# Kernel tuning notes

Hardware: AMD Instinct MI355X
Metric: run time of the kernel (lower is better)

## Reference

```python
import jax, jax.numpy as jnp
import numpy as np

N_NODES = 50000
BN_EPS = 1e-5


def gcn_conv(x, W, b, src, dst):
    # PyG GCNConv: linear, add self-loops, symmetric degree normalization, scatter-add, bias.
    h = x @ W                                        # [N, D]
    n = x.shape[0]
    deg = jax.ops.segment_sum(jnp.ones(src.shape[0], x.dtype), dst,
                              num_segments=n) + 1.0  # +1 for self-loop
    dinv = jnp.where(deg > 0, jax.lax.rsqrt(deg), 0.0)
    norm = dinv[src] * dinv[dst]                     # [E]
    agg = jax.ops.segment_sum(h[src] * norm[:, None], dst, num_segments=n)
    agg = agg + h * (dinv * dinv)[:, None]           # self-loop contribution
    return agg + b


def batch_norm(x, gamma, beta):
    # training-mode BN over the node axis (biased variance, as torch)
    mu = jnp.mean(x, axis=0)
    var = jnp.mean((x - mu) ** 2, axis=0)
    return (x - mu) * jax.lax.rsqrt(var + BN_EPS) * gamma + beta


def setup_inputs() -> dict:
    key = jax.random.key(0)
    ks = jax.random.split(key, 8)
    D, C = 128, 10
    x = jax.random.normal(ks[0], (N_NODES, D), dtype=jnp.float32)
    edge_index = jax.random.randint(ks[1], (2, 640000), 0, N_NODES, dtype=jnp.int32)
    s = 1.0 / np.sqrt(D)
    return {
        "x": x,
        "edge_index": edge_index,
        "W1": jax.random.normal(ks[2], (D, D), dtype=jnp.float32) * s,
        "b1": jnp.zeros((D,), jnp.float32),
        "gamma1": jnp.ones((D,), jnp.float32),
        "beta1": jnp.zeros((D,), jnp.float32),
        "W2": jax.random.normal(ks[3], (D, D), dtype=jnp.float32) * s,
        "b2": jnp.zeros((D,), jnp.float32),
        "gamma2": jnp.ones((D,), jnp.float32),
        "beta2": jnp.zeros((D,), jnp.float32),
        "lin1_w": jax.random.normal(ks[4], (D, D), dtype=jnp.float32) * s,
        "lin1_b": jnp.zeros((D,), jnp.float32),
        "lin2_w": jax.random.normal(ks[5], (D, C), dtype=jnp.float32) * s,
        "lin2_b": jnp.zeros((C,), jnp.float32),
    }


def reference(x, edge_index, W1, b1, gamma1, beta1, W2, b2, gamma2, beta2,
              lin1_w, lin1_b, lin2_w, lin2_b):
    src, dst = edge_index[0], edge_index[1]
    # layer 1: GCNConv -> ReLU -> BN (dropout = identity at eval)
    h = jax.nn.relu(gcn_conv(x, W1, b1, src, dst))
    h = batch_norm(h, gamma1, beta1)
    # layer 2
    h = jax.nn.relu(gcn_conv(h, W2, b2, src, dst))
    h = batch_norm(h, gamma2, beta2)
    # MLP head
    h = jax.nn.relu(h @ lin1_w + lin1_b)
    logits = h @ lin2_w + lin2_b
    return jax.nn.log_softmax(logits, axis=-1)
```

## Files before the change

kernel.cpp:

```cpp
#include <hip/hip_runtime.h>
#include <hip/hip_bf16.h>
#include <math.h>

typedef unsigned int uint;
typedef unsigned short ushort;
using f32x4 = __attribute__((ext_vector_type(4))) float;
using s16x8 = __attribute__((ext_vector_type(8))) short;

#define NSLOT 64

__device__ __forceinline__ float bflo(uint u) { return __uint_as_float(u << 16); }
__device__ __forceinline__ float bfhi(uint u) { return __uint_as_float(u & 0xffff0000u); }
__device__ __forceinline__ ushort f2bf(float f) {
    uint u = __float_as_uint(f);
    return (ushort)((u + 0x7fffu + ((u >> 16) & 1u)) >> 16);
}
__device__ __forceinline__ float sel4f(float a, float b, float c, float d, int i) {
    float r = a; r = (i == 1) ? b : r; r = (i == 2) ? c : r; r = (i == 3) ? d : r; return r;
}
__device__ __forceinline__ int sel4i(int a, int b, int c, int d, int i) {
    int r = a; r = (i == 1) ? b : r; r = (i == 2) ? c : r; r = (i == 3) ? d : r; return r;
}


__global__ __launch_bounds__(256) void init_prep(uint4* __restrict__ zbase, int nz, int ZB,
                                                 const float* __restrict__ W1,
                                                 const float* __restrict__ W2,
                                                 const float* __restrict__ W3,
                                                 const float* __restrict__ l2w,
                                                 const float* __restrict__ l2b,
                                                 ushort* __restrict__ wt1,
                                                 ushort* __restrict__ wt2,
                                                 ushort* __restrict__ wt3,
                                                 ushort* __restrict__ w2bf,
                                                 float* __restrict__ b2pad) {
    int bid = blockIdx.x;
    if (bid < ZB) {
        int i = bid * 256 + threadIdx.x;
        if (i < nz) zbase[i] = (uint4){0u, 0u, 0u, 0u};
        return;
    }
    int i = (bid - ZB) * 256 + threadIdx.x;
    int li = i & 16383;
    int k = li >> 7, n = li & 127;
    const float* Ws = (i < 16384) ? W1 : (i < 32768) ? W2 : W3;
    ushort* Wd = (i < 16384) ? wt1 : (i < 32768) ? wt2 : wt3;
    Wd[n * 128 + k] = f2bf(Ws[li]);
    if (i < 2048) {
        int c = i >> 7, kk = i & 127;
        float v = (c < 10) ? l2w[kk * 10 + c] : 0.f;
        w2bf[c * 128 + kk] = f2bf(v);
    }
    if (i < 16) b2pad[i] = (i < 10) ? l2b[i] : -1e30f;
}


__global__ __launch_bounds__(256) void deg_count(const int* __restrict__ dst,
                                                 int* __restrict__ deg, int E) {
    int base = blockIdx.x * 1024 + threadIdx.x;
    int d[4]; bool ok[4];
    #pragma unroll
    for (int k = 0; k < 4; ++k) {
        int e = base + k * 256;
        ok[k] = e < E;
        d[k] = ok[k] ? dst[e] : 0;
    }
    #pragma unroll
    for (int k = 0; k < 4; ++k)
        if (ok[k]) atomicAdd(&deg[d[k]], 1);
}


__global__ __launch_bounds__(256) void scan_fill(const int* __restrict__ deg,
                                                 int* __restrict__ bsum,
                                                 int* __restrict__ sync_ctr,
                                                 int* __restrict__ row_start,
                                                 int* __restrict__ cursor,
                                                 float* __restrict__ dinv,
                                                 int N, int E, int nblk) {
    __shared__ int s[256];
    __shared__ int sb[256];
    int t = threadIdx.x;
    int bid = blockIdx.x;
    int i = bid * 256 + t;
    int dg = (i < N) ? deg[i] : 0;
    s[t] = dg;
    __syncthreads();
    for (int off = 1; off < 256; off <<= 1) {
        int v = (t >= off) ? s[t - off] : 0;
        __syncthreads();
        s[t] += v;
        __syncthreads();
    }
    if (t == 0) {
        bsum[bid] = s[255];
        __threadfence();
        atomicAdd(sync_ctr, 1);
        while (atomicAdd(sync_ctr, 0) < nblk) __builtin_amdgcn_s_sleep(8);
    }
    __syncthreads();
    sb[t] = (t < nblk) ? atomicAdd(&bsum[t], 0) : 0;
    __syncthreads();
    for (int off = 1; off < 256; off <<= 1) {
        int v = (t >= off) ? sb[t - off] : 0;
        __syncthreads();
        sb[t] += v;
        __syncthreads();
    }
    if (i < N) {
        int boff = (bid == 0) ? 0 : sb[bid - 1];
        int excl = boff + s[t] - dg;
        row_start[i] = excl;
        cursor[i] = excl;
        dinv[i] = rsqrtf((float)dg + 1.0f);
    }
    if (i == 0) row_start[N] = E;
}


__global__ __launch_bounds__(256) void csr_fill(const int* __restrict__ src,
                                                const int* __restrict__ dst,
                                                int* __restrict__ cursor,
                                                int* __restrict__ csr_src, int E) {
    int base = blockIdx.x * 1024 + threadIdx.x;
    int s[4], d[4]; bool ok[4];
    #pragma unroll
    for (int k = 0; k < 4; ++k) {
        int e = base + k * 256;
        ok[k] = e < E;
        s[k] = ok[k] ? src[e] : 0;
        d[k] = ok[k] ? dst[e] : 0;
    }
    #pragma unroll
    for (int k = 0; k < 4; ++k) {
        if (ok[k]) {
            int p = atomicAdd(&cursor[d[k]], 1);
            csr_src[p] = s[k];
        }
    }
}


template<bool XF32, bool AFF, bool PRESCALE, bool HEAD>
__global__ __launch_bounds__(256) void gemm_mfma(const void* __restrict__ Xv,
                                                 const float* __restrict__ scale,
                                                 const float* __restrict__ shift,
                                                 const ushort* __restrict__ Bt,
                                                 const float* __restrict__ bias,
                                                 const float* __restrict__ dinv,
                                                 ushort* __restrict__ Y,
                                                 const ushort* __restrict__ W2bf,
                                                 const float* __restrict__ b2pad,
                                                 float* __restrict__ OUT, int N) {
    __shared__ char smem[2 * 16384 + 32768];
    char* Bl = smem + 32768;

    int tid = threadIdx.x;
    int brow = blockIdx.x * 128;

    {
        int n = tid >> 1, h = tid & 1;
        const uint4* srcp = (const uint4*)(Bt + n * 128 + h * 64);
        #pragma unroll
        for (int i = 0; i < 8; ++i) {
            uint4 v = srcp[i];
            int u = (h * 8 + i) ^ (n & 7);
            *(uint4*)(Bl + n * 256 + u * 16) = v;
        }
    }

    int lane = tid & 63, w = tid >> 6;
    int m = lane & 15, g = lane >> 4;
    int wr = w * 16;

    #pragma unroll
    for (int t = 0; t < 2; ++t) {
        char* Al = smem + t * 16384;
        int rbase = brow + t * 64;

        {
            int r = tid >> 2, c0 = (tid & 3) * 32;
            int row = rbase + r;
            bool ok = row < N;
            uint pk[16];
            if (XF32) {
                const float* Xr = (const float*)Xv + (size_t)row * 128 + c0;
                #pragma unroll
                for (int i = 0; i < 16; ++i) {
                    float f0 = ok ? Xr[i * 2] : 0.f;
                    float f1 = ok ? Xr[i * 2 + 1] : 0.f;
                    pk[i] = (uint)f2bf(f0) | ((uint)f2bf(f1) << 16);
                }
            } else {
                const uint* Xr = (const uint*)((const ushort*)Xv + (size_t)row * 128 + c0);
                #pragma unroll
                for (int i = 0; i < 16; ++i) {
                    uint u = ok ? Xr[i] : 0u;
                    float f0 = bflo(u), f1 = bfhi(u);
                    if (AFF) {
                        int c = c0 + i * 2;
                        f0 = f0 * scale[c] + shift[c];
                        f1 = f1 * scale[c + 1] + shift[c + 1];
                    }
                    pk[i] = (uint)f2bf(f0) | ((uint)f2bf(f1) << 16);
                }
            }
            #pragma unroll
            for (int i = 0; i < 4; ++i) {
                int u = ((tid & 3) * 4 + i) ^ (r & 7);
                *(uint4*)(Al + r * 256 + u * 16) = *(uint4*)&pk[i * 4];
            }
        }
        __syncthreads();

        f32x4 acc[8];
        #pragma unroll
        for (int nt = 0; nt < 8; ++nt) acc[nt] = (f32x4){0.f, 0.f, 0.f, 0.f};

        #pragma unroll
        for (int kk = 0; kk < 4; ++kk) {
            int u = (kk * 4 + g) ^ (m & 7);
            s16x8 a = *(const s16x8*)(Al + (wr + m) * 256 + u * 16);
            #pragma unroll
            for (int nt = 0; nt < 8; ++nt) {
                s16x8 b = *(const s16x8*)(Bl + (nt * 16 + m) * 256 + u * 16);
                acc[nt] = __builtin_amdgcn_mfma_f32_16x16x32_bf16(a, b, acc[nt], 0, 0, 0);
            }
        }

        if (!HEAD) {
            #pragma unroll
            for (int i = 0; i < 4; ++i) {
                int row = rbase + wr + g * 4 + i;
                if (row < N) {
                    float dv = PRESCALE ? dinv[row] : 1.f;
                    #pragma unroll
                    for (int nt = 0; nt < 8; ++nt) {
                        float v = acc[nt][i];
                        if (PRESCALE) v *= dv;
                        Y[(size_t)row * 128 + nt * 16 + m] = f2bf(v);
                    }
                }
            }
        } else {
            float bv[8];
            #pragma unroll
            for (int nt = 0; nt < 8; ++nt) bv[nt] = bias[nt * 16 + m];
            #pragma unroll
            for (int i = 0; i < 4; ++i) {
                int r = wr + g * 4 + i;
                #pragma unroll
                for (int nt = 0; nt < 8; ++nt) {
                    float v = fmaxf(acc[nt][i] + bv[nt], 0.f);
                    int col = nt * 16 + m;
                    int u = (col >> 3) ^ (r & 7);
                    *(ushort*)(Al + r * 256 + u * 16 + (col & 7) * 2) = f2bf(v);
                }
            }
            __syncthreads();
            float b2v = b2pad[m];
            f32x4 lg = (f32x4){b2v, b2v, b2v, b2v};
            #pragma unroll
            for (int kk = 0; kk < 4; ++kk) {
                int u = (kk * 4 + g) ^ (m & 7);
                s16x8 a = *(const s16x8*)(Al + (wr + m) * 256 + u * 16);
                s16x8 b = *(const s16x8*)(&W2bf[m * 128 + (kk * 4 + g) * 8]);
                lg = __builtin_amdgcn_mfma_f32_16x16x32_bf16(a, b, lg, 0, 0, 0);
            }
            #pragma unroll
            for (int i = 0; i < 4; ++i) {
                float v = lg[i];
                float mx = v;
                #pragma unroll
                for (int off = 8; off > 0; off >>= 1) mx = fmaxf(mx, __shfl_xor(mx, off, 64));
                float ex = expf(v - mx);
                float sm = ex;
                #pragma unroll
                for (int off = 8; off > 0; off >>= 1) sm += __shfl_xor(sm, off, 64);
                float res = v - (mx + logf(sm));
                int grow = rbase + wr + g * 4 + i;
                if (m < 10 && grow < N) OUT[(size_t)grow * 10 + m] = res;
            }
        }
    }
}


__global__ __launch_bounds__(256) void gather_fused(const ushort* __restrict__ H,
                                                    const int* __restrict__ row_start,
                                                    const int* __restrict__ csr_src,
                                                    const float* __restrict__ dinv,
                                                    const float* __restrict__ bias,
                                                    ushort* __restrict__ Y,
                                                    float* __restrict__ bnpart, int N) {
    int g = threadIdx.x >> 6, lane = threadIdx.x & 63;
    int d = lane * 2;
    float b0 = bias[d], b1 = bias[d + 1];
    float s0 = 0.f, s1 = 0.f, ss0 = 0.f, ss1 = 0.f;

    int nchunks = (N + 3) / 4;
    int chunk = blockIdx.x * 4 + g;

    if (chunk < nchunks) {
        int c = chunk * 4;
        int nn = min(4, N - c);

        int rsv = row_start[c + min(lane, nn)];
        int rs0 = __shfl(rsv, 0);
        int rs1 = __shfl(rsv, min(1, nn));
        int rs2 = __shfl(rsv, min(2, nn));
        int rs3 = __shfl(rsv, min(3, nn));
        int rs4 = __shfl(rsv, nn);

        float dvv = dinv[c + min(lane, nn - 1)];
        float dv0 = __shfl(dvv, 0);
        float dv1 = __shfl(dvv, min(1, nn - 1));
        float dv2 = __shfl(dvv, min(2, nn - 1));
        float dv3 = __shfl(dvv, min(3, nn - 1));

        uint h0 = *(const uint*)&H[(size_t)c * 128 + d];
        uint h1 = (nn > 1) ? *(const uint*)&H[(size_t)(c + 1) * 128 + d] : 0u;
        uint h2 = (nn > 2) ? *(const uint*)&H[(size_t)(c + 2) * 128 + d] : 0u;
        uint h3 = (nn > 3) ? *(const uint*)&H[(size_t)(c + 3) * 128 + d] : 0u;

        float i0_0 = bflo(h0) * dv0 + b0, i1_0 = bfhi(h0) * dv0 + b1;
        float i0_1 = bflo(h1) * dv1 + b0, i1_1 = bfhi(h1) * dv1 + b1;
        float i0_2 = bflo(h2) * dv2 + b0, i1_2 = bfhi(h2) * dv2 + b1;
        float i0_3 = bflo(h3) * dv3 + b0, i1_3 = bfhi(h3) * dv3 + b1;

        int e0 = rs0, eend = rs4;
        int seg = 0;
        int nextb = rs1;
        float i0s = i0_0, i1s = i1_0, dvs = dv0;
        float es0 = 0.f, es1 = 0.f;

        for (int base = e0; base < eend; base += 64) {
            int cnt = min(64, eend - base);
            int sl = (lane < cnt) ? csr_src[base + lane] : 0;

            for (int j = 0; j < cnt; j += 16) {
                int mm = min(16, cnt - j);
                uint v[16];
                #pragma unroll
                for (int k = 0; k < 16; ++k) {
                    int idx = min(j + k, cnt - 1);
                    int sk = __shfl(sl, idx);
                    v[k] = *(const uint*)&H[(size_t)sk * 128 + d];
                }
                #pragma unroll
                for (int k = 0; k < 16; ++k) {
                    if (k < mm) {
                        int e = base + j + k;
                        while (e >= nextb) {
                            float r0 = fmaxf(es0 * dvs + i0s, 0.f);
                            float r1 = fmaxf(es1 * dvs + i1s, 0.f);
                            *(uint*)&Y[(size_t)(c + seg) * 128 + d] =
                                (uint)f2bf(r0) | ((uint)f2bf(r1) << 16);
                            s0 += r0; ss0 += r0 * r0; s1 += r1; ss1 += r1 * r1;
                            seg++;
                            i0s = sel4f(i0_0, i0_1, i0_2, i0_3, seg);
                            i1s = sel4f(i1_0, i1_1, i1_2, i1_3, seg);
                            dvs = sel4f(dv0, dv1, dv2, dv3, seg);
                            nextb = sel4i(rs1, rs2, rs3, rs4, seg);
                            es0 = 0.f; es1 = 0.f;
                        }
                        es0 += bflo(v[k]);
                        es1 += bfhi(v[k]);
                    }
                }
            }
        }
        for (;;) {
            float r0 = fmaxf(es0 * dvs + i0s, 0.f);
            float r1 = fmaxf(es1 * dvs + i1s, 0.f);
            *(uint*)&Y[(size_t)(c + seg) * 128 + d] = (uint)f2bf(r0) | ((uint)f2bf(r1) << 16);
            s0 += r0; ss0 += r0 * r0; s1 += r1; ss1 += r1 * r1;
            seg++;
            if (seg >= nn) break;
            i0s = sel4f(i0_0, i0_1, i0_2, i0_3, seg);
            i1s = sel4f(i1_0, i1_1, i1_2, i1_3, seg);
            dvs = sel4f(dv0, dv1, dv2, dv3, seg);
            nextb = sel4i(rs1, rs2, rs3, rs4, seg);
            es0 = 0.f; es1 = 0.f;
        }
    }

    float* bp = bnpart + (size_t)(blockIdx.x & (NSLOT - 1)) * 256;
    __shared__ float red[4][128];
    red[g][d] = s0; red[g][d + 1] = s1;
    __syncthreads();
    if (g == 0) {
        atomicAdd(&bp[d],     red[0][d] + red[1][d] + red[2][d] + red[3][d]);
        atomicAdd(&bp[d + 1], red[0][d + 1] + red[1][d + 1] + red[2][d + 1] + red[3][d + 1]);
    }
    __syncthreads();
    red[g][d] = ss0; red[g][d + 1] = ss1;
    __syncthreads();
    if (g == 0) {
        atomicAdd(&bp[128 + d],     red[0][d] + red[1][d] + red[2][d] + red[3][d]);
        atomicAdd(&bp[128 + d + 1], red[0][d + 1] + red[1][d + 1] + red[2][d + 1] + red[3][d + 1]);
    }
}

__global__ void bnfinalize(float* __restrict__ bnpart,
                           const float* __restrict__ gamma, const float* __restrict__ beta,
                           float* __restrict__ scale, float* __restrict__ shift, float invN) {
    int d = threadIdx.x;
    float sum = 0.f, ss = 0.f;
    #pragma unroll 8
    for (int s = 0; s < NSLOT; ++s) {
        sum += bnpart[s * 256 + d];
        ss  += bnpart[s * 256 + 128 + d];
        bnpart[s * 256 + d] = 0.f;
        bnpart[s * 256 + 128 + d] = 0.f;
    }
    float mu  = sum * invN;
    float var = ss * invN - mu * mu;
    float sc  = gamma[d] * rsqrtf(var + 1e-5f);
    scale[d] = sc;
    shift[d] = beta[d] - mu * sc;
}


static inline char* align16(char* p) { return (char*)(((uintptr_t)p + 15) & ~(uintptr_t)15); }

extern "C" void kernel_launch(void* const* d_in, const int* in_sizes, int n_in,
                              void* d_out, int out_size, void* d_ws, size_t ws_size,
                              hipStream_t stream) {
    const float* x    = (const float*)d_in[0];
    const int*   ei   = (const int*)d_in[1];
    const float* W1   = (const float*)d_in[2];
    const float* b1   = (const float*)d_in[3];
    const float* g1   = (const float*)d_in[4];
    const float* be1  = (const float*)d_in[5];
    const float* W2   = (const float*)d_in[6];
    const float* b2   = (const float*)d_in[7];
    const float* g2   = (const float*)d_in[8];
    const float* be2  = (const float*)d_in[9];
    const float* l1w  = (const float*)d_in[10];
    const float* l1b  = (const float*)d_in[11];
    const float* l2w  = (const float*)d_in[12];
    const float* l2b  = (const float*)d_in[13];
    float* out = (float*)d_out;

    int N = in_sizes[0] / 128;
    int E = in_sizes[1] / 2;
    const int* srcp = ei;
    const int* dstp = ei + E;

    char* w = (char*)d_ws;
    ushort* bufA   = (ushort*)w;  w = align16(w + (size_t)N * 128 * 2);
    ushort* bufB   = (ushort*)w;  w = align16(w + (size_t)N * 128 * 2);
    char* zstart   = w;
    int*   degc    = (int*)w;     w += (size_t)N * 4;
    float* bnpart  = (float*)w;   w += (size_t)NSLOT * 256 * 4;
    int*   ctrs    = (int*)w;     w += 16;
    size_t zbytes  = (size_t)(w - zstart);
    w = align16(w);
    float* dinv    = (float*)w;   w = align16(w + (size_t)N * 4);
    int*   row_st  = (int*)w;     w = align16(w + (size_t)(N + 1) * 4);
    int*   cursor  = (int*)w;     w = align16(w + (size_t)N * 4);
    int*   bsum    = (int*)w;     w = align16(w + 256 * 4);
    int*   csr_src = (int*)w;     w = align16(w + (size_t)E * 4);
    float* scale   = (float*)w;   w = align16(w + 128 * 4);
    float* shift   = (float*)w;   w = align16(w + 128 * 4);
    ushort* wt1    = (ushort*)w;  w = align16(w + 16384 * 2);
    ushort* wt2    = (ushort*)w;  w = align16(w + 16384 * 2);
    ushort* wt3    = (ushort*)w;  w = align16(w + 16384 * 2);
    ushort* w2bf   = (ushort*)w;  w = align16(w + 2048 * 2);
    float* b2pad   = (float*)w;   w = align16(w + 16 * 4);

    int nz = (int)(zbytes / 16);
    int ZB = (nz + 255) / 256;
    int eg4 = (E + 1023) / 1024;
    int ng = (N + 255) / 256;
    int gemm_grid = (N + 127) / 128;
    int nchunks = (N + 3) / 4;
    int gather_grid = (nchunks + 3) / 4;
    float invN = 1.0f / (float)N;

    init_prep<<<ZB + 192, 256, 0, stream>>>((uint4*)zstart, nz, ZB,
                                            W1, W2, l1w, l2w, l2b, wt1, wt2, wt3, w2bf, b2pad);
    deg_count<<<eg4, 256, 0, stream>>>(dstp, degc, E);
    scan_fill<<<ng, 256, 0, stream>>>(degc, bsum, &ctrs[0], row_st, cursor, dinv, N, E, ng);
    csr_fill<<<eg4, 256, 0, stream>>>(srcp, dstp, cursor, csr_src, E);

    gemm_mfma<true, false, true, false><<<gemm_grid, 256, 0, stream>>>(
        x, nullptr, nullptr, wt1, nullptr, dinv, bufA, nullptr, nullptr, nullptr, N);
    gather_fused<<<gather_grid, 256, 0, stream>>>(bufA, row_st, csr_src, dinv, b1, bufB, bnpart, N);
    bnfinalize<<<1, 128, 0, stream>>>(bnpart, g1, be1, scale, shift, invN);

    gemm_mfma<false, true, true, false><<<gemm_grid, 256, 0, stream>>>(
        bufB, scale, shift, wt2, nullptr, dinv, bufA, nullptr, nullptr, nullptr, N);
    gather_fused<<<gather_grid, 256, 0, stream>>>(bufA, row_st, csr_src, dinv, b2, bufB, bnpart, N);
    bnfinalize<<<1, 128, 0, stream>>>(bnpart, g2, be2, scale, shift, invN);

    gemm_mfma<false, true, false, true><<<gemm_grid, 256, 0, stream>>>(
        bufB, scale, shift, wt3, l1b, nullptr, nullptr, w2bf, b2pad, out, N);
}
```

Baseline: 327.4 us.

## Fold BN finalize into GEMM prologue and make gather persistent with atomic work counter

Removes the two single-block bnfinalize launches. Each GEMM block now reduces the BN partial sums into shared-memory scale and shift itself, and separate partial buffers per layer replace the in-kernel zeroing. The gather kernel becomes persistent: a fixed grid of 1024 blocks where each wave claims node chunks through an atomic counter instead of one chunk per wave. NSLOT is halved to cut the redundant per-block reduction, at the cost of more atomic contention on the partial sums and one counter atomic per chunk.

```diff
diff --git a/kernel.cpp b/kernel.cpp
--- a/kernel.cpp
+++ b/kernel.cpp
@@ -7,7 +7,7 @@
 using f32x4 = __attribute__((ext_vector_type(4))) float;
 using s16x8 = __attribute__((ext_vector_type(8))) short;
 
-#define NSLOT 64
+#define NSLOT 32
 
 __device__ __forceinline__ float bflo(uint u) { return __uint_as_float(u << 16); }
 __device__ __forceinline__ float bfhi(uint u) { return __uint_as_float(u & 0xffff0000u); }
@@ -143,8 +143,10 @@
 
 template<bool XF32, bool AFF, bool PRESCALE, bool HEAD>
 __global__ __launch_bounds__(256) void gemm_mfma(const void* __restrict__ Xv,
-                                                 const float* __restrict__ scale,
-                                                 const float* __restrict__ shift,
+                                                 const float* __restrict__ bnp,
+                                                 const float* __restrict__ gamma,
+                                                 const float* __restrict__ beta,
+                                                 float invN,
                                                  const ushort* __restrict__ Bt,
                                                  const float* __restrict__ bias,
                                                  const float* __restrict__ dinv,
@@ -153,10 +155,27 @@
                                                  const float* __restrict__ b2pad,
                                                  float* __restrict__ OUT, int N) {
     __shared__ char smem[2 * 16384 + 32768];
+    __shared__ float sscale[128], sshift[128];
     char* Bl = smem + 32768;
 
     int tid = threadIdx.x;
     int brow = blockIdx.x * 128;
+
+    if (AFF) {
+        if (tid < 128) {
+            float sum = 0.f, ss = 0.f;
+            #pragma unroll 8
+            for (int s = 0; s < NSLOT; ++s) {
+                sum += bnp[s * 256 + tid];
+                ss  += bnp[s * 256 + 128 + tid];
+            }
+            float mu  = sum * invN;
+            float var = ss * invN - mu * mu;
+            float sc  = gamma[tid] * rsqrtf(var + 1e-5f);
+            sscale[tid] = sc;
+            sshift[tid] = beta[tid] - mu * sc;
+        }
+    }
 
     {
         int n = tid >> 1, h = tid & 1;
@@ -168,6 +187,7 @@
             *(uint4*)(Bl + n * 256 + u * 16) = v;
         }
     }
+    __syncthreads();
 
     int lane = tid & 63, w = tid >> 6;
     int m = lane & 15, g = lane >> 4;
@@ -199,8 +219,8 @@
                     float f0 = bflo(u), f1 = bfhi(u);
                     if (AFF) {
                         int c = c0 + i * 2;
-                        f0 = f0 * scale[c] + shift[c];
-                        f1 = f1 * scale[c + 1] + shift[c + 1];
+                        f0 = f0 * sscale[c] + sshift[c];
+                        f1 = f1 * sscale[c + 1] + sshift[c + 1];
                     }
                     pk[i] = (uint)f2bf(f0) | ((uint)f2bf(f1) << 16);
                 }
@@ -292,16 +312,21 @@
                                                     const float* __restrict__ dinv,
                                                     const float* __restrict__ bias,
                                                     ushort* __restrict__ Y,
-                                                    float* __restrict__ bnpart, int N) {
+                                                    float* __restrict__ bnpart,
+                                                    int* __restrict__ wctr, int N) {
     int g = threadIdx.x >> 6, lane = threadIdx.x & 63;
     int d = lane * 2;
     float b0 = bias[d], b1 = bias[d + 1];
     float s0 = 0.f, s1 = 0.f, ss0 = 0.f, ss1 = 0.f;
 
     int nchunks = (N + 3) / 4;
-    int chunk = blockIdx.x * 4 + g;
-
-    if (chunk < nchunks) {
+
+    for (;;) {
+        int chunk = 0;
+        if (lane == 0) chunk = atomicAdd(wctr, 1);
+        chunk = __shfl(chunk, 0);
+        if (chunk >= nchunks) break;
+
         int c = chunk * 4;
         int nn = min(4, N - c);
 
@@ -402,25 +427,6 @@
     }
 }
 
-__global__ void bnfinalize(float* __restrict__ bnpart,
-                           const float* __restrict__ gamma, const float* __restrict__ beta,
-                           float* __restrict__ scale, float* __restrict__ shift, float invN) {
-    int d = threadIdx.x;
-    float sum = 0.f, ss = 0.f;
-    #pragma unroll 8
-    for (int s = 0; s < NSLOT; ++s) {
-        sum += bnpart[s * 256 + d];
-        ss  += bnpart[s * 256 + 128 + d];
-        bnpart[s * 256 + d] = 0.f;
-        bnpart[s * 256 + 128 + d] = 0.f;
-    }
-    float mu  = sum * invN;
-    float var = ss * invN - mu * mu;
-    float sc  = gamma[d] * rsqrtf(var + 1e-5f);
-    scale[d] = sc;
-    shift[d] = beta[d] - mu * sc;
-}
-
 
 static inline char* align16(char* p) { return (char*)(((uintptr_t)p + 15) & ~(uintptr_t)15); }
 
@@ -453,7 +459,8 @@
     ushort* bufB   = (ushort*)w;  w = align16(w + (size_t)N * 128 * 2);
     char* zstart   = w;
     int*   degc    = (int*)w;     w += (size_t)N * 4;
-    float* bnpart  = (float*)w;   w += (size_t)NSLOT * 256 * 4;
+    float* bnpA    = (float*)w;   w += (size_t)NSLOT * 256 * 4;
+    float* bnpB    = (float*)w;   w += (size_t)NSLOT * 256 * 4;
     int*   ctrs    = (int*)w;     w += 16;
     size_t zbytes  = (size_t)(w - zstart);
     w = align16(w);
@@ -462,8 +469,6 @@
     int*   cursor  = (int*)w;     w = align16(w + (size_t)N * 4);
     int*   bsum    = (int*)w;     w = align16(w + 256 * 4);
     int*   csr_src = (int*)w;     w = align16(w + (size_t)E * 4);
-    float* scale   = (float*)w;   w = align16(w + 128 * 4);
-    float* shift   = (float*)w;   w = align16(w + 128 * 4);
     ushort* wt1    = (ushort*)w;  w = align16(w + 16384 * 2);
     ushort* wt2    = (ushort*)w;  w = align16(w + 16384 * 2);
     ushort* wt3    = (ushort*)w;  w = align16(w + 16384 * 2);
@@ -475,8 +480,7 @@
     int eg4 = (E + 1023) / 1024;
     int ng = (N + 255) / 256;
     int gemm_grid = (N + 127) / 128;
-    int nchunks = (N + 3) / 4;
-    int gather_grid = (nchunks + 3) / 4;
+    int gather_grid = 1024;
     float invN = 1.0f / (float)N;
 
     init_prep<<<ZB + 192, 256, 0, stream>>>((uint4*)zstart, nz, ZB,
@@ -486,15 +490,15 @@
     csr_fill<<<eg4, 256, 0, stream>>>(srcp, dstp, cursor, csr_src, E);
 
     gemm_mfma<true, false, true, false><<<gemm_grid, 256, 0, stream>>>(
-        x, nullptr, nullptr, wt1, nullptr, dinv, bufA, nullptr, nullptr, nullptr, N);
-    gather_fused<<<gather_grid, 256, 0, stream>>>(bufA, row_st, csr_src, dinv, b1, bufB, bnpart, N);
-    bnfinalize<<<1, 128, 0, stream>>>(bnpart, g1, be1, scale, shift, invN);
+        x, nullptr, nullptr, nullptr, 0.f, wt1, nullptr, dinv, bufA, nullptr, nullptr, nullptr, N);
+    gather_fused<<<gather_grid, 256, 0, stream>>>(bufA, row_st, csr_src, dinv, b1, bufB,
+                                                  bnpA, &ctrs[1], N);
 
     gemm_mfma<false, true, true, false><<<gemm_grid, 256, 0, stream>>>(
-        bufB, scale, shift, wt2, nullptr, dinv, bufA, nullptr, nullptr, nullptr, N);
-    gather_fused<<<gather_grid, 256, 0, stream>>>(bufA, row_st, csr_src, dinv, b2, bufB, bnpart, N);
-    bnfinalize<<<1, 128, 0, stream>>>(bnpart, g2, be2, scale, shift, invN);
+        bufB, bnpA, g1, be1, invN, wt2, nullptr, dinv, bufA, nullptr, nullptr, nullptr, N);
+    gather_fused<<<gather_grid, 256, 0, stream>>>(bufA, row_st, csr_src, dinv, b2, bufB,
+                                                  bnpB, &ctrs[2], N);
 
     gemm_mfma<false, true, false, true><<<gemm_grid, 256, 0, stream>>>(
-        bufB, scale, shift, wt3, l1b, nullptr, nullptr, w2bf, b2pad, out, N);
-}
+        bufB, bnpB, g2, be2, invN, wt3, l1b, nullptr, nullptr, w2bf, b2pad, out, N);
+}
```

New measurement: 633.8 us. 93.6% more time.
